# Optimization experiments

Measured on AMD Instinct MI355X. Metric: run time of the kernel, lower is better.

Reference implementation:

```python
import jax, jax.numpy as jnp
import numpy as np
import math

EMBED_DIM = 128
NUM_HEADS = 8
HDIM = EMBED_DIM // NUM_HEADS


def setup_inputs() -> dict:
    key = jax.random.key(0)
    kq, kh, km, k1, k2, k3, k4 = jax.random.split(key, 7)
    B, NQ, GS = 32, 1024, 1024
    q = jax.random.normal(kq, (B, NQ, EMBED_DIM), dtype=jnp.float32)
    h = jax.random.normal(kh, (B, GS, EMBED_DIM), dtype=jnp.float32)
    mask = jax.random.bernoulli(km, 0.15, (B, NQ, GS))
    stdv = 1.0 / math.sqrt(HDIM)
    Wq = jax.random.uniform(k1, (NUM_HEADS, EMBED_DIM, HDIM), jnp.float32, -stdv, stdv)
    Wk = jax.random.uniform(k2, (NUM_HEADS, EMBED_DIM, HDIM), jnp.float32, -stdv, stdv)
    Wv = jax.random.uniform(k3, (NUM_HEADS, EMBED_DIM, HDIM), jnp.float32, -stdv, stdv)
    stdv_o = 1.0 / math.sqrt(EMBED_DIM)
    Wout = jax.random.uniform(k4, (NUM_HEADS, HDIM, EMBED_DIM), jnp.float32, -stdv_o, stdv_o)
    return {"q": q, "h": h, "mask": mask, "Wq": Wq, "Wk": Wk, "Wv": Wv, "Wout": Wout}


def reference(q, h, mask, Wq, Wk, Wv, Wout):
    norm = 1.0 / math.sqrt(HDIM)
    # per-head projections: [h, b, n, e]
    Q = jnp.einsum('bnd,hde->hbne', q, Wq)
    K = jnp.einsum('bgd,hde->hbge', h, Wk)
    V = jnp.einsum('bgd,hde->hbge', h, Wv)
    compat = norm * jnp.einsum('hbne,hbge->hbng', Q, K)  # [h,b,nq,gs]
    m = mask[None]  # broadcast over heads
    compat = jnp.where(m, -jnp.inf, compat)
    attn = jax.nn.softmax(compat, axis=-1)
    attn = jnp.where(m, 0.0, attn)
    heads = jnp.einsum('hbng,hbge->hbne', attn, V)
    out = jnp.einsum('hbne,hed->bnd', heads, Wout)
    return out
```

## Files before the change

### kernel.cpp

```cpp
#include <hip/hip_runtime.h>

typedef unsigned short u16;
typedef unsigned int   u32;
typedef short bf16x8 __attribute__((ext_vector_type(8)));
typedef float f32x2  __attribute__((ext_vector_type(2)));
typedef float f32x4  __attribute__((ext_vector_type(4)));
typedef float f32x16 __attribute__((ext_vector_type(16)));

#define NB  32
#define NQ  1024
#define GS  1024
#define NH  8
#define SCQ (0.25f * 1.4426950408889634f)
#define MBIG (-1.0e30f)

#define MFMA16(a, b, c) __builtin_amdgcn_mfma_f32_16x16x32_bf16(a, b, c, 0, 0, 0)
#define MFMA32(a, b, c) __builtin_amdgcn_mfma_f32_32x32x16_bf16(a, b, c, 0, 0, 0)

__device__ __forceinline__ u16 f2bf(float f) {
    u32 u = __float_as_uint(f);
    return (u16)((u + 0x7fffu + ((u >> 16) & 1u)) >> 16);
}
__device__ __forceinline__ u32 pk2bf(float a, float b) {
    u32 ua = __float_as_uint(a) + 0x8000u;
    u32 ub = __float_as_uint(b) + 0x8000u;
    return __builtin_amdgcn_perm(ub, ua, 0x07060302u);
}

__global__ __launch_bounds__(256) void wprep(const float* __restrict__ Wq,
                                             const float* __restrict__ Wk,
                                             const float* __restrict__ Wv,
                                             const float* __restrict__ Wout,
                                             u16* __restrict__ Wp) {
    int g = blockIdx.x * 256 + threadIdx.x;
    int m = g >> 14;
    int i = g & 16383;
    const float* src = (m == 0) ? Wq : (m == 1) ? Wk : (m == 2) ? Wv : Wout;
    float sc = (m == 0) ? SCQ : 1.0f;
    float v;
    if (m < 3) { int cc = i >> 7, k = i & 127;  v = src[(cc >> 4) * 2048 + k * 16 + (cc & 15)]; }
    else       { int d  = i >> 7, he = i & 127; v = src[(he >> 4) * 2048 + (he & 15) * 128 + d]; }
    Wp[m * 16384 + i] = f2bf(v * sc);
}

template <int MODE>
__device__ __forceinline__ void mgemm(const float* __restrict__ Ain,
                                      const u16* __restrict__ Wpm,
                                      u16* __restrict__ outb,
                                      u16* As, u16* Ws, int row0) {
    const int t    = threadIdx.x;
    const int wv   = t >> 6;
    const int lane = t & 63;
    const int quad = lane >> 4;
    const int c    = lane & 15;

#pragma unroll
    for (int g0 = 0; g0 < 2048; g0 += 256) {
        int g = g0 + t;
        int row = g >> 4, k0 = (g & 15) * 8;
        const float4* ap = (const float4*)&Ain[(size_t)(row0 + row) * 128 + k0];
        float4 a0 = ap[0], a1 = ap[1];
        int4 pk;
        pk.x = (int)pk2bf(a0.x, a0.y);
        pk.y = (int)pk2bf(a0.z, a0.w);
        pk.z = (int)pk2bf(a1.x, a1.y);
        pk.w = (int)pk2bf(a1.z, a1.w);
        *(int4*)&As[row * 136 + k0] = pk;
    }
#pragma unroll
    for (int g0 = 0; g0 < 2048; g0 += 256) {
        int g = g0 + t;
        int cc = g >> 4, k0 = (g & 15) * 8;
        *(int4*)&Ws[cc * 136 + k0] = *(const int4*)&Wpm[cc * 128 + k0];
    }
    __syncthreads();

    const f32x4 zf = {0.f, 0.f, 0.f, 0.f};
    f32x4 acc[2][8];
#pragma unroll
    for (int s = 0; s < 2; ++s)
#pragma unroll
        for (int j = 0; j < 8; ++j) acc[s][j] = zf;

#pragma unroll
    for (int kt = 0; kt < 4; ++kt) {
        bf16x8 af0 = *(const bf16x8*)&As[(wv * 32 + c) * 136 + kt * 32 + quad * 8];
        bf16x8 af1 = *(const bf16x8*)&As[(wv * 32 + 16 + c) * 136 + kt * 32 + quad * 8];
#pragma unroll
        for (int j = 0; j < 8; ++j) {
            bf16x8 bfr = *(const bf16x8*)&Ws[(j * 16 + c) * 136 + kt * 32 + quad * 8];
            acc[0][j] = MFMA16(af0, bfr, acc[0][j]);
            acc[1][j] = MFMA16(af1, bfr, acc[1][j]);
        }
    }

    __syncthreads();
    u16* Os = As;
#pragma unroll
    for (int s = 0; s < 2; ++s)
#pragma unroll
        for (int j = 0; j < 8; ++j)
#pragma unroll
            for (int r = 0; r < 4; ++r) {
                int lrow = wv * 32 + s * 16 + quad * 4 + r;
                int col  = j * 16 + c;
                u16 v = f2bf(acc[s][j][r]);
                if (MODE == 0) {
                    Os[lrow * 136 + col] = v;
                } else {
                    Os[col * 136 + lrow] = v;
                }
            }
    __syncthreads();

    if (MODE == 0) {
#pragma unroll
        for (int it = 0; it < 8; ++it) {
            int chunk = it * 256 + t;
            int lrow = chunk >> 4, c0 = (chunk & 15) * 8;
            *(int4*)&outb[(size_t)(row0 + lrow) * 128 + c0] =
                *(const int4*)&Os[lrow * 136 + c0];
        }
    } else {
        int bI = row0 >> 10, tb0 = row0 & 1023;
#pragma unroll
        for (int it = 0; it < 8; ++it) {
            int chunk = it * 256 + t;
            int col = chunk >> 4, t0 = (chunk & 15) * 8;
            *(int4*)&outb[(size_t)bI * (128 * 1024) + (size_t)col * 1024 + tb0 + t0] =
                *(const int4*)&Os[col * 136 + t0];
        }
    }
}

__global__ __launch_bounds__(256, 2) void proj_mfma(const float* __restrict__ q,
                                                    const float* __restrict__ h,
                                                    const u16* __restrict__ Wp,
                                                    u16* __restrict__ Qb,
                                                    u16* __restrict__ Kb,
                                                    u16* __restrict__ Vtg) {
    __shared__ u16 As[128 * 136];
    __shared__ u16 Ws[128 * 136];
    int row0 = blockIdx.x * 128;
    if (blockIdx.y == 0)      mgemm<0>(q, Wp,         Qb,  As, Ws, row0);
    else if (blockIdx.y == 1) mgemm<0>(h, Wp + 16384, Kb,  As, Ws, row0);
    else                      mgemm<2>(h, Wp + 32768, Vtg, As, Ws, row0);
}

__global__ __launch_bounds__(512, 4) void flash_mfma(const u16* __restrict__ Qb,
                                                     const u16* __restrict__ Kb,
                                                     const u16* __restrict__ Vtg,
                                                     const int* __restrict__ mask,
                                                     const u16* __restrict__ Wob,
                                                     float* __restrict__ out) {
    __shared__ u16 Kt[64 * 136];
    __shared__ u16 Vtt[128 * 72];
    __shared__ u16 Ps[NH][64 * 36];
    __shared__ float Mf[32 * 68];

    const int b    = blockIdx.x;
    const int q0   = blockIdx.y * 32;
    const int t    = threadIdx.x;
    const int hh   = t >> 6;
    const int lane = t & 63;
    const int quad = lane >> 4;
    const int c    = lane & 15;
    const int qq   = lane & 31;
    const int hi   = lane >> 5;

    const f32x4 zf = {0.f, 0.f, 0.f, 0.f};

    bf16x8 qf = *(const bf16x8*)&Qb[((size_t)b * NQ + q0 + qq) * 128 +
                                    hh * 16 + hi * 8];

    f32x4 O[2] = {zf, zf};
    float lsum = 0.f;

    const int skey = t >> 4;
    const int sd0  = (t & 15) * 8;
    const int vdim = t >> 2;
    const int vs0  = (t & 3) * 8;
    const int mrow = t >> 4;
    const int mk0  = (t & 15) * 2;

    const u16* Kptr = &Kb[((size_t)b * GS + skey) * 128 + sd0];
    const u16* Vptr = &Vtg[(size_t)b * (128 * 1024) + (size_t)vdim * 1024 + vs0];
    const int* Mptr = &mask[((size_t)b * NQ + q0 + mrow) * GS + mk0];

    int4 kreg0 = *(const int4*)Kptr;
    int4 kreg1 = *(const int4*)(Kptr + 32 * 128);
    int4 vreg0 = *(const int4*)Vptr;
    int4 vreg1 = *(const int4*)(Vptr + 32);
    int2 mreg0 = *(const int2*)Mptr;
    int2 mreg1 = *(const int2*)(Mptr + 32);

    for (int g0 = 0; g0 < GS; g0 += 64) {
        __syncthreads();
        *(int4*)&Kt[skey * 136 + sd0]        = kreg0;
        *(int4*)&Kt[(32 + skey) * 136 + sd0] = kreg1;
        *(int4*)&Vtt[vdim * 72 + vs0]        = vreg0;
        *(int4*)&Vtt[vdim * 72 + 32 + vs0]   = vreg1;
        f32x2 mm0, mm1;
        mm0.x = mreg0.x ? MBIG : 0.f;
        mm0.y = mreg0.y ? MBIG : 0.f;
        mm1.x = mreg1.x ? MBIG : 0.f;
        mm1.y = mreg1.y ? MBIG : 0.f;
        *(f32x2*)&Mf[mrow * 68 + mk0]      = mm0;
        *(f32x2*)&Mf[mrow * 68 + 32 + mk0] = mm1;
        __syncthreads();

        if (g0 + 64 < GS) {
            Kptr += 64 * 128;
            kreg0 = *(const int4*)Kptr;
            kreg1 = *(const int4*)(Kptr + 32 * 128);
            Vptr += 64;
            vreg0 = *(const int4*)Vptr;
            vreg1 = *(const int4*)(Vptr + 32);
            Mptr += 64;
            mreg0 = *(const int2*)Mptr;
            mreg1 = *(const int2*)(Mptr + 32);
        }

        bf16x8 kf0 = *(const bf16x8*)&Kt[qq * 136 + hh * 16 + hi * 8];
        bf16x8 kf1 = *(const bf16x8*)&Kt[(32 + qq) * 136 + hh * 16 + hi * 8];
        bf16x8 vf0 = *(const bf16x8*)&Vtt[(hh * 16 + c) * 72 + quad * 8];
        bf16x8 vf1 = *(const bf16x8*)&Vtt[(hh * 16 + c) * 72 + 32 + quad * 8];
        f32x16 c0, c1;
#pragma unroll
        for (int blk = 0; blk < 4; ++blk) {
            f32x4 m0 = *(const f32x4*)&Mf[qq * 68 + 8 * blk + 4 * hi];
            f32x4 m1 = *(const f32x4*)&Mf[qq * 68 + 32 + 8 * blk + 4 * hi];
            c0[4 * blk + 0] = m0.x;  c0[4 * blk + 1] = m0.y;
            c0[4 * blk + 2] = m0.z;  c0[4 * blk + 3] = m0.w;
            c1[4 * blk + 0] = m1.x;  c1[4 * blk + 1] = m1.y;
            c1[4 * blk + 2] = m1.z;  c1[4 * blk + 3] = m1.w;
        }
        f32x16 sc0 = MFMA32(kf0, qf, c0);
        f32x16 sc1 = MFMA32(kf1, qf, c1);

        float e0[16];
#pragma unroll
        for (int r = 0; r < 16; ++r) e0[r] = __builtin_amdgcn_exp2f(sc0[r]);
        lsum += ((e0[0] + e0[1]) + (e0[2] + e0[3])) + ((e0[4] + e0[5]) + (e0[6] + e0[7])) +
                (((e0[8] + e0[9]) + (e0[10] + e0[11])) + ((e0[12] + e0[13]) + (e0[14] + e0[15])));
#pragma unroll
        for (int blk = 0; blk < 4; ++blk) {
            int2 pw;
            pw.x = (int)pk2bf(e0[4 * blk + 0], e0[4 * blk + 1]);
            pw.y = (int)pk2bf(e0[4 * blk + 2], e0[4 * blk + 3]);
            *(int2*)&Ps[hh][qq * 36 + 8 * blk + 4 * hi] = pw;
        }

        float e1[16];
#pragma unroll
        for (int r = 0; r < 16; ++r) e1[r] = __builtin_amdgcn_exp2f(sc1[r]);
        lsum += ((e1[0] + e1[1]) + (e1[2] + e1[3])) + ((e1[4] + e1[5]) + (e1[6] + e1[7])) +
                (((e1[8] + e1[9]) + (e1[10] + e1[11])) + ((e1[12] + e1[13]) + (e1[14] + e1[15])));
#pragma unroll
        for (int blk = 0; blk < 4; ++blk) {
            int2 pw;
            pw.x = (int)pk2bf(e1[4 * blk + 0], e1[4 * blk + 1]);
            pw.y = (int)pk2bf(e1[4 * blk + 2], e1[4 * blk + 3]);
            *(int2*)&Ps[hh][1152 + qq * 36 + 8 * blk + 4 * hi] = pw;
        }

#pragma unroll
        for (int s = 0; s < 2; ++s) {
            bf16x8 pf = *(const bf16x8*)&Ps[hh][(s * 16 + c) * 36 + quad * 8];
            O[s] = MFMA16(pf, vf0, O[s]);
        }
#pragma unroll
        for (int s = 0; s < 2; ++s) {
            bf16x8 pf = *(const bf16x8*)&Ps[hh][1152 + (s * 16 + c) * 36 + quad * 8];
            O[s] = MFMA16(pf, vf1, O[s]);
        }
    }

    lsum += __shfl_xor(lsum, 32);
    float rlv = (lsum > 0.f) ? 1.f / lsum : 0.f;

    __syncthreads();
    u16* Hs = Kt;
#pragma unroll
    for (int s = 0; s < 2; ++s)
#pragma unroll
        for (int r = 0; r < 4; ++r) {
            float rlq = __shfl(rlv, s * 16 + quad * 4 + r);
            Hs[(s * 16 + quad * 4 + r) * 136 + hh * 16 + c] =
                f2bf(O[s][r] * rlq);
        }
    __syncthreads();

    f32x4 oacc[2] = {zf, zf};
#pragma unroll
    for (int kt = 0; kt < 4; ++kt) {
        bf16x8 bfr = *(const bf16x8*)&Wob[(hh * 16 + c) * 128 + kt * 32 + quad * 8];
#pragma unroll
        for (int s = 0; s < 2; ++s) {
            bf16x8 af = *(const bf16x8*)&Hs[(s * 16 + c) * 136 + kt * 32 + quad * 8];
            oacc[s] = MFMA16(af, bfr, oacc[s]);
        }
    }
#pragma unroll
    for (int s = 0; s < 2; ++s)
#pragma unroll
        for (int r = 0; r < 4; ++r)
            out[((size_t)b * NQ + q0 + s * 16 + quad * 4 + r) * 128 + hh * 16 + c] =
                oacc[s][r];
}

extern "C" void kernel_launch(void* const* d_in, const int* in_sizes, int n_in,
                              void* d_out, int out_size, void* d_ws, size_t ws_size,
                              hipStream_t stream) {
    const float* q    = (const float*)d_in[0];
    const float* h    = (const float*)d_in[1];
    const int*   mask = (const int*)d_in[2];
    const float* Wq   = (const float*)d_in[3];
    const float* Wk   = (const float*)d_in[4];
    const float* Wv   = (const float*)d_in[5];
    const float* Wout = (const float*)d_in[6];
    float* out = (float*)d_out;

    const size_t NTOK = (size_t)NB * NQ;
    u16* Qb  = (u16*)d_ws;
    u16* Kb  = Qb + NTOK * 128;
    u16* Vtg = Kb + NTOK * 128;
    u16* Wp  = Vtg + NTOK * 128;

    wprep<<<dim3(256), 256, 0, stream>>>(Wq, Wk, Wv, Wout, Wp);
    proj_mfma<<<dim3(256, 3), 256, 0, stream>>>(q, h, Wp, Qb, Kb, Vtg);
    flash_mfma<<<dim3(NB, NQ / 32), 512, 0, stream>>>(Qb, Kb, Vtg, mask,
                                                      Wp + 49152, out);
}
```

Before: 275.4 us.

## Fuse weight prep into projection kernel and load activations straight to registers

Removes the separate wprep launch. Each projection block now converts and transposes its raw fp32 weight matrix into LDS, and a fourth grid row converts Wout for the attention kernel. Activation fragments are loaded from global memory directly into registers as bf16 instead of staging through an LDS tile. This halves LDS use so occupancy can rise to 3 blocks per CU, at the cost of redundant weight conversion per block and scattered 2-byte LDS stores.

```diff
diff --git a/kernel.cpp b/kernel.cpp
--- a/kernel.cpp
+++ b/kernel.cpp
@@ -27,27 +27,12 @@
     return __builtin_amdgcn_perm(ub, ua, 0x07060302u);
 }
 
-__global__ __launch_bounds__(256) void wprep(const float* __restrict__ Wq,
-                                             const float* __restrict__ Wk,
-                                             const float* __restrict__ Wv,
-                                             const float* __restrict__ Wout,
-                                             u16* __restrict__ Wp) {
-    int g = blockIdx.x * 256 + threadIdx.x;
-    int m = g >> 14;
-    int i = g & 16383;
-    const float* src = (m == 0) ? Wq : (m == 1) ? Wk : (m == 2) ? Wv : Wout;
-    float sc = (m == 0) ? SCQ : 1.0f;
-    float v;
-    if (m < 3) { int cc = i >> 7, k = i & 127;  v = src[(cc >> 4) * 2048 + k * 16 + (cc & 15)]; }
-    else       { int d  = i >> 7, he = i & 127; v = src[(he >> 4) * 2048 + (he & 15) * 128 + d]; }
-    Wp[m * 16384 + i] = f2bf(v * sc);
-}
-
 template <int MODE>
 __device__ __forceinline__ void mgemm(const float* __restrict__ Ain,
-                                      const u16* __restrict__ Wpm,
+                                      const float* __restrict__ Wraw,
+                                      float wsc,
                                       u16* __restrict__ outb,
-                                      u16* As, u16* Ws, int row0) {
+                                      u16* Ws, int row0) {
     const int t    = threadIdx.x;
     const int wv   = t >> 6;
     const int lane = t & 63;
@@ -56,22 +41,39 @@
 
 #pragma unroll
     for (int g0 = 0; g0 < 2048; g0 += 256) {
-        int g = g0 + t;
-        int row = g >> 4, k0 = (g & 15) * 8;
-        const float4* ap = (const float4*)&Ain[(size_t)(row0 + row) * 128 + k0];
-        float4 a0 = ap[0], a1 = ap[1];
-        int4 pk;
-        pk.x = (int)pk2bf(a0.x, a0.y);
-        pk.y = (int)pk2bf(a0.z, a0.w);
-        pk.z = (int)pk2bf(a1.x, a1.y);
-        pk.w = (int)pk2bf(a1.z, a1.w);
-        *(int4*)&As[row * 136 + k0] = pk;
-    }
-#pragma unroll
-    for (int g0 = 0; g0 < 2048; g0 += 256) {
-        int g = g0 + t;
-        int cc = g >> 4, k0 = (g & 15) * 8;
-        *(int4*)&Ws[cc * 136 + k0] = *(const int4*)&Wpm[cc * 128 + k0];
+        int idx  = g0 + t;
+        int hk   = idx >> 1, half = idx & 1;
+        int k    = hk & 127;
+        int col0 = (hk >> 7) * 16 + half * 8;
+        const float4* wp = (const float4*)&Wraw[hk * 16 + half * 8];
+        float4 w0 = wp[0], w1 = wp[1];
+        Ws[(col0 + 0) * 136 + k] = f2bf(w0.x * wsc);
+        Ws[(col0 + 1) * 136 + k] = f2bf(w0.y * wsc);
+        Ws[(col0 + 2) * 136 + k] = f2bf(w0.z * wsc);
+        Ws[(col0 + 3) * 136 + k] = f2bf(w0.w * wsc);
+        Ws[(col0 + 4) * 136 + k] = f2bf(w1.x * wsc);
+        Ws[(col0 + 5) * 136 + k] = f2bf(w1.y * wsc);
+        Ws[(col0 + 6) * 136 + k] = f2bf(w1.z * wsc);
+        Ws[(col0 + 7) * 136 + k] = f2bf(w1.w * wsc);
+    }
+
+    const float* a0p = &Ain[(size_t)(row0 + wv * 32 + c) * 128];
+    const float* a1p = &Ain[(size_t)(row0 + wv * 32 + 16 + c) * 128];
+    bf16x8 af0[4], af1[4];
+#pragma unroll
+    for (int kt = 0; kt < 4; ++kt) {
+        int k0 = kt * 32 + quad * 8;
+        float4 x0 = *(const float4*)&a0p[k0];
+        float4 x1 = *(const float4*)&a0p[k0 + 4];
+        float4 y0 = *(const float4*)&a1p[k0];
+        float4 y1 = *(const float4*)&a1p[k0 + 4];
+        int4 p0, p1;
+        p0.x = (int)pk2bf(x0.x, x0.y);  p0.y = (int)pk2bf(x0.z, x0.w);
+        p0.z = (int)pk2bf(x1.x, x1.y);  p0.w = (int)pk2bf(x1.z, x1.w);
+        p1.x = (int)pk2bf(y0.x, y0.y);  p1.y = (int)pk2bf(y0.z, y0.w);
+        p1.z = (int)pk2bf(y1.x, y1.y);  p1.w = (int)pk2bf(y1.z, y1.w);
+        __builtin_memcpy(&af0[kt], &p0, 16);
+        __builtin_memcpy(&af1[kt], &p1, 16);
     }
     __syncthreads();
 
@@ -84,18 +86,16 @@
 
 #pragma unroll
     for (int kt = 0; kt < 4; ++kt) {
-        bf16x8 af0 = *(const bf16x8*)&As[(wv * 32 + c) * 136 + kt * 32 + quad * 8];
-        bf16x8 af1 = *(const bf16x8*)&As[(wv * 32 + 16 + c) * 136 + kt * 32 + quad * 8];
 #pragma unroll
         for (int j = 0; j < 8; ++j) {
             bf16x8 bfr = *(const bf16x8*)&Ws[(j * 16 + c) * 136 + kt * 32 + quad * 8];
-            acc[0][j] = MFMA16(af0, bfr, acc[0][j]);
-            acc[1][j] = MFMA16(af1, bfr, acc[1][j]);
-        }
-    }
-
-    __syncthreads();
-    u16* Os = As;
+            acc[0][j] = MFMA16(af0[kt], bfr, acc[0][j]);
+            acc[1][j] = MFMA16(af1[kt], bfr, acc[1][j]);
+        }
+    }
+
+    __syncthreads();
+    u16* Os = Ws;
 #pragma unroll
     for (int s = 0; s < 2; ++s)
 #pragma unroll
@@ -133,18 +133,30 @@
     }
 }
 
-__global__ __launch_bounds__(256, 2) void proj_mfma(const float* __restrict__ q,
+__global__ __launch_bounds__(256, 3) void proj_mfma(const float* __restrict__ q,
                                                     const float* __restrict__ h,
-                                                    const u16* __restrict__ Wp,
+                                                    const float* __restrict__ Wq,
+                                                    const float* __restrict__ Wk,
+                                                    const float* __restrict__ Wv,
+                                                    const float* __restrict__ Wout,
                                                     u16* __restrict__ Qb,
                                                     u16* __restrict__ Kb,
-                                                    u16* __restrict__ Vtg) {
-    __shared__ u16 As[128 * 136];
+                                                    u16* __restrict__ Vtg,
+                                                    u16* __restrict__ Wob) {
     __shared__ u16 Ws[128 * 136];
+    int y = blockIdx.y;
+    if (y == 3) {
+        if (blockIdx.x < 64) {
+            int i = blockIdx.x * 256 + threadIdx.x;
+            int d = i >> 7, he = i & 127;
+            Wob[i] = f2bf(Wout[(he >> 4) * 2048 + (he & 15) * 128 + d]);
+        }
+        return;
+    }
     int row0 = blockIdx.x * 128;
-    if (blockIdx.y == 0)      mgemm<0>(q, Wp,         Qb,  As, Ws, row0);
-    else if (blockIdx.y == 1) mgemm<0>(h, Wp + 16384, Kb,  As, Ws, row0);
-    else                      mgemm<2>(h, Wp + 32768, Vtg, As, Ws, row0);
+    if (y == 0)      mgemm<0>(q, Wq, SCQ,  Qb,  Ws, row0);
+    else if (y == 1) mgemm<0>(h, Wk, 1.0f, Kb,  Ws, row0);
+    else             mgemm<2>(h, Wv, 1.0f, Vtg, Ws, row0);
 }
 
 __global__ __launch_bounds__(512, 4) void flash_mfma(const u16* __restrict__ Qb,
@@ -325,10 +337,10 @@
     u16* Qb  = (u16*)d_ws;
     u16* Kb  = Qb + NTOK * 128;
     u16* Vtg = Kb + NTOK * 128;
-    u16* Wp  = Vtg + NTOK * 128;
-
-    wprep<<<dim3(256), 256, 0, stream>>>(Wq, Wk, Wv, Wout, Wp);
-    proj_mfma<<<dim3(256, 3), 256, 0, stream>>>(q, h, Wp, Qb, Kb, Vtg);
+    u16* Wob = Vtg + NTOK * 128;
+
+    proj_mfma<<<dim3(256, 4), 256, 0, stream>>>(q, h, Wq, Wk, Wv, Wout,
+                                                Qb, Kb, Vtg, Wob);
     flash_mfma<<<dim3(NB, NQ / 32), 512, 0, stream>>>(Qb, Kb, Vtg, mask,
-                                                      Wp + 49152, out);
-}
+                                                      Wob, out);
+}
```

Result: no change. 275.3 us (-0.0%).
